# Performance work log

Hardware: AMD Instinct MI355X
Metric: run time of the kernel (lower is better)

The kernel has to match this reference:

```python
import jax, jax.numpy as jnp
import numpy as np

S, M, B, D, H, DH = 1024, 1024, 4, 1024, 16, 64
T = S + M
EPS = 1e-5


def setup_inputs() -> dict:
    key = jax.random.key(0)
    ks = jax.random.split(key, 6)
    x = jax.random.normal(ks[0], (S, B, D), dtype=jnp.float32)
    pos_emb = jax.random.normal(ks[1], (S, 1, D), dtype=jnp.float32)
    memory = jax.random.normal(ks[2], (M, B, D), dtype=jnp.float32)
    # causal mask: query i (global position M+i) cannot attend to key j > M+i
    i = jnp.arange(S)[:, None]
    j = jnp.arange(T)[None, :]
    mask = jnp.broadcast_to((j > (i + M))[:, :, None], (S, T, B))  # [S,T,B] bool
    w_qkv = jax.random.normal(ks[3], (D, 3 * H * DH), dtype=jnp.float32) * (D ** -0.5)
    w_o = jax.random.normal(ks[4], (H * DH, D), dtype=jnp.float32) * ((H * DH) ** -0.5)
    ln_gamma = jnp.ones((D,), dtype=jnp.float32)
    ln_beta = jnp.zeros((D,), dtype=jnp.float32)
    return {"x": x, "pos_emb": pos_emb, "memory": memory, "mask": mask,
            "w_qkv": w_qkv, "w_o": w_o, "ln_gamma": ln_gamma, "ln_beta": ln_beta}


def reference(x, pos_emb, memory, mask, w_qkv, w_o, ln_gamma, ln_beta):
    seq_len = x.shape[0]
    scale = 1.0 / (DH ** 0.5)
    x = x + pos_emb[-seq_len:]                      # [S,B,D]
    c = jnp.concatenate([memory, x], axis=0)        # [T,B,D]
    qkv = jnp.einsum('tbd,de->tbe', c, w_qkv)       # [T,B,3*H*DH]
    q, k, v = jnp.split(qkv, 3, axis=-1)
    q = q.reshape(-1, B, H, DH)[-seq_len:]          # [S,B,H,DH]
    k = k.reshape(-1, B, H, DH)                     # [T,B,H,DH]
    v = v.reshape(-1, B, H, DH)
    score = jnp.einsum('ibnd,jbnd->ijbn', q, k) * scale  # [S,T,B,H]
    score = jnp.where(mask[:, :, :, None], -jnp.inf, score)
    prob = jax.nn.softmax(score, axis=1)
    vec = jnp.einsum('ijbn,jbnd->ibnd', prob, v)    # [S,B,H,DH]
    vec = vec.reshape(seq_len, B, H * DH)
    attn_out = jnp.einsum('sbe,ed->sbd', vec, w_o)  # [S,B,D]
    y = x + attn_out
    mu = jnp.mean(y, axis=-1, keepdims=True)
    var = jnp.mean(jnp.square(y - mu), axis=-1, keepdims=True)
    out = (y - mu) * jax.lax.rsqrt(var + EPS) * ln_gamma + ln_beta
    return out
```

## Files before the change

### kernel.cpp

```cpp
#include <hip/hip_runtime.h>
#include <stdint.h>

#define S_  1024
#define M_  1024
#define B_  4
#define D_  1024
#define H_  16
#define DH_ 64
#define T_  2048

typedef __attribute__((ext_vector_type(8))) short bf8;
typedef __attribute__((ext_vector_type(4))) float f32x4;
typedef __attribute__((ext_vector_type(16))) float f32x16;
typedef __attribute__((ext_vector_type(8))) unsigned short u16x8;
typedef __attribute__((ext_vector_type(4))) unsigned short u16x4;
typedef __attribute__((ext_vector_type(4))) unsigned int u32x4;
typedef unsigned short u16;

#define MFMA(a, b, c)   __builtin_amdgcn_mfma_f32_16x16x32_bf16((a), (b), (c), 0, 0, 0)
#define MFMA32(a, b, c) __builtin_amdgcn_mfma_f32_32x32x16_bf16((a), (b), (c), 0, 0, 0)

#define SIG(r) ((((r) >> 1) ^ ((r) >> 3)) & 3)

static __device__ __forceinline__ u16 f2bf(float f) {
  unsigned int u = __builtin_bit_cast(unsigned int, f);
  u += 0x7fffu + ((u >> 16) & 1u);
  return (u16)(u >> 16);
}

static __device__ __forceinline__ void gload16(const void* g, void* l) {
  __builtin_amdgcn_global_load_lds((const __attribute__((address_space(1))) unsigned int*)g,
                                   (__attribute__((address_space(3))) unsigned int*)l,
                                   16, 0, 0);
}

static __device__ __forceinline__ float fexp2(float x) {
  return __builtin_amdgcn_exp2f(x);
}
static __device__ __forceinline__ unsigned int cvtpk(float lo, float hi) {
  unsigned int r; asm("v_cvt_pk_bf16_f32 %0, %1, %2" : "=v"(r) : "v"(lo), "v"(hi)); return r;
}
static __device__ __forceinline__ void plswap(unsigned int& a, unsigned int& b) {
  asm volatile("s_nop 1\n\tv_permlane32_swap_b32 %0, %1" : "+v"(a), "+v"(b));
}

__global__ __launch_bounds__(256) void k_prep(const float* __restrict__ x,
    const float* __restrict__ pos, const float* __restrict__ mem,
    u16* __restrict__ cbf, float* __restrict__ xp)
{
  const int gid = blockIdx.x * 256 + threadIdx.x;
  const int e = gid * 8;
  const int row = e >> 10, col = e & 1023;
  float4 v0, v1;
  if (e < M_ * B_ * D_) {
    v0 = *(const float4*)(mem + e);
    v1 = *(const float4*)(mem + e + 4);
  } else {
    const int i2 = e - M_ * B_ * D_;
    v0 = *(const float4*)(x + i2);
    v1 = *(const float4*)(x + i2 + 4);
    const int srow = i2 >> 12;
    const float4 p0 = *(const float4*)(pos + srow * 1024 + col);
    const float4 p1 = *(const float4*)(pos + srow * 1024 + col + 4);
    v0.x += p0.x; v0.y += p0.y; v0.z += p0.z; v0.w += p0.w;
    v1.x += p1.x; v1.y += p1.y; v1.z += p1.z; v1.w += p1.w;
    *(float4*)(xp + i2) = v0;
    *(float4*)(xp + i2 + 4) = v1;
  }
  u16x8 c;
  c[0] = f2bf(v0.x); c[1] = f2bf(v0.y); c[2] = f2bf(v0.z); c[3] = f2bf(v0.w);
  c[4] = f2bf(v1.x); c[5] = f2bf(v1.y); c[6] = f2bf(v1.z); c[7] = f2bf(v1.w);
  const int ch = col >> 3;
  const int chs = (ch & ~3) | ((ch & 3) ^ SIG(row));
  *(u16x8*)(cbf + (size_t)row * 1024 + chs * 8) = c;
}

__global__ __launch_bounds__(256) void k_wtrans(const float* __restrict__ src,
    u16* __restrict__ dst, int Rr, int Cc, int swz)
{
  __shared__ float tl[64][65];
  const int r0 = blockIdx.x * 64, c0 = blockIdx.y * 64;
  const int tid = threadIdx.x;
  const int lr = tid >> 4, lc = (tid & 15) * 4;
  for (int i = 0; i < 4; ++i) {
    const int rr = lr + i * 16;
    const float4 v = *(const float4*)(src + (size_t)(r0 + rr) * Cc + c0 + lc);
    tl[rr][lc] = v.x; tl[rr][lc + 1] = v.y; tl[rr][lc + 2] = v.z; tl[rr][lc + 3] = v.w;
  }
  __syncthreads();
  const int c = tid >> 2, k0 = (tid & 3) * 16;
  u16x8 a, b;
  for (int j = 0; j < 8; ++j) { a[j] = f2bf(tl[k0 + j][c]); b[j] = f2bf(tl[k0 + 8 + j][c]); }
  const int roww = c0 + c;
  int ch0 = (r0 + k0) >> 3, ch1 = ((r0 + k0) >> 3) + 1;
  if (swz) {
    const int sx = SIG(roww);
    ch0 = (ch0 & ~3) | ((ch0 & 3) ^ sx);
    ch1 = (ch1 & ~3) | ((ch1 & 3) ^ sx);
  }
  u16* dp = dst + (size_t)roww * Rr;
  *(u16x8*)(dp + ch0 * 8) = a;
  *(u16x8*)(dp + ch1 * 8) = b;
}

__global__ __launch_bounds__(256, 3) void k_gemm_qkvs(const u16* __restrict__ A,
    const u16* __restrict__ Bt, u16* __restrict__ Qd, u16* __restrict__ Kd,
    u16* __restrict__ VTd)
{
  __shared__ u16 sA[3][4096];
  __shared__ u16 sB[3][4096];
  const int tid = threadIdx.x, lane = tid & 63, wave = tid >> 6;
  const int lrow = lane & 15, lgrp = lane >> 4;
  const int wm = (wave >> 1) * 64, wn = (wave & 1) * 64;
  const int sr = lane >> 2, sk = (lane & 3) * 8;

  const int bid = blockIdx.x;
  const int lid = (bid & 7) * 160 + (bid >> 3);
  int rowb, colb;
  if (lid < 512) { rowb = lid >> 4; colb = 8 + (lid & 15); }
  else { const int l2 = lid - 512; const int q = l2 / 24; rowb = 32 + q; colb = l2 - q * 24; }
  const int row0 = rowb * 128, col0 = colb * 128;

  f32x4 acc[4][4];
#pragma unroll
  for (int i = 0; i < 4; ++i)
#pragma unroll
    for (int j = 0; j < 4; ++j) acc[i][j] = f32x4{0.f, 0.f, 0.f, 0.f};

#define STAGE_S(bufi, kt) do { const int k0_ = (kt) * 32;                      \
    _Pragma("unroll") for (int s_ = 0; s_ < 2; ++s_) {                         \
      const int rr_ = (wave * 2 + s_) * 16 + sr;                               \
      gload16(A + (size_t)(row0 + rr_) * 1024 + k0_ + sk,                      \
              &sA[bufi][(wave * 2 + s_) * 512]);                               \
      gload16(Bt + (size_t)(col0 + rr_) * 1024 + k0_ + sk,                     \
              &sB[bufi][(wave * 2 + s_) * 512]);                               \
    } } while (0)

  STAGE_S(0, 0); STAGE_S(1, 1);

  int c0 = 0;
#pragma unroll 1
  for (int t = 0; t < 32; ++t) {
    if (t < 31) { asm volatile("s_waitcnt vmcnt(4)" ::: "memory"); }
    else        { asm volatile("s_waitcnt vmcnt(0)" ::: "memory"); }
    __builtin_amdgcn_s_barrier();
    __builtin_amdgcn_sched_barrier(0);
    const int c2 = (c0 + 2 >= 3) ? c0 - 1 : c0 + 2;
    if (t <= 29) STAGE_S(c2, t + 2);
    bf8 af[4], bfv[4];
#pragma unroll
    for (int i = 0; i < 4; ++i) {
      const int r_ = wm + i * 16 + lrow;
      af[i] = *(const bf8*)&sA[c0][r_ * 32 + ((lgrp ^ SIG(r_)) << 3)];
    }
#pragma unroll
    for (int j = 0; j < 4; ++j) {
      const int r_ = wn + j * 16 + lrow;
      bfv[j] = *(const bf8*)&sB[c0][r_ * 32 + ((lgrp ^ SIG(r_)) << 3)];
    }
    __builtin_amdgcn_s_setprio(1);
#pragma unroll
    for (int i = 0; i < 4; ++i)
#pragma unroll
      for (int j = 0; j < 4; ++j) acc[i][j] = MFMA(af[i], bfv[j], acc[i][j]);
    __builtin_amdgcn_s_setprio(0);
    c0 = (c0 == 2) ? 0 : c0 + 1;
  }

  const int which = col0 >> 10;
#pragma unroll
  for (int i = 0; i < 4; ++i)
#pragma unroll
    for (int j = 0; j < 4; ++j)
#pragma unroll
      for (int r = 0; r < 4; ++r) {
        const int grow = row0 + wm + i * 16 + lgrp * 4 + r;
        const int gcol = col0 + wn + j * 16 + lrow;
        const u16 bv = f2bf(acc[i][j][r]);
        const int t = grow >> 2, bb2 = grow & 3;
        const int rem = gcol & 1023;
        const int bh = bb2 * 16 + (rem >> 6), dh = rem & 63;
        if (which == 0) {
          if (t >= M_) Qd[((size_t)bh * S_ + (t - M_)) * 64 + dh] = bv;
        } else if (which == 1) {
          Kd[((size_t)bh * T_ + t) * 64 + (dh ^ ((t & 7) << 3))] = bv;
        } else {
          VTd[((size_t)bh * 64 + dh) * T_ + (t & ~63) + ((t & 63) ^ ((dh & 7) << 3))] = bv;
        }
      }
}

__global__ __launch_bounds__(256) void k_gemm_out(const u16* __restrict__ A,
    const u16* __restrict__ Bt, const float* __restrict__ xp,
    float* __restrict__ y)
{
  __shared__ u16 sA[2][2048];
  __shared__ u16 sB[2][4096];
  const int tid = threadIdx.x, lane = tid & 63, wave = tid >> 6;
  const int lrow = lane & 15, lgrp = lane >> 4;
  const int wm = (wave >> 1) * 32, wn = (wave & 1) * 64;
  const int row0 = blockIdx.y * 64, col0 = blockIdx.x * 128;
  const int sr = lane >> 2, sk = (lane & 3) * 8;

  f32x4 acc[2][4];
  for (int i = 0; i < 2; ++i)
    for (int j = 0; j < 4; ++j) acc[i][j] = f32x4{0.f, 0.f, 0.f, 0.f};

#define STAGE_O(buf, kt) do { const int k0_ = (kt) * 32;                       \
    const int rra_ = wave * 16 + sr;                                           \
    gload16(A + (size_t)(row0 + rra_) * 1024 + k0_ + sk,                       \
            &sA[buf][wave * 512]);                                             \
    for (int s_ = 0; s_ < 2; ++s_) {                                           \
      const int rrb_ = (wave * 2 + s_) * 16 + sr;                              \
      gload16(Bt + (size_t)(col0 + rrb_) * 1024 + k0_ + sk,                    \
              &sB[buf][(wave * 2 + s_) * 512]);                                \
    } } while (0)

  STAGE_O(0, 0);
  int cur = 0;
  for (int kt = 0; kt < 32; ++kt) {
    asm volatile("s_waitcnt vmcnt(0)" ::: "memory");
    __syncthreads();
    if (kt + 1 < 32) STAGE_O(cur ^ 1, kt + 1);
    bf8 af[2], bfv[4];
    const u16* pa = &sA[cur][(wm + lrow) * 32 + lgrp * 8];
    const u16* pb = &sB[cur][(wn + lrow) * 32 + lgrp * 8];
    for (int i = 0; i < 2; ++i) af[i] = *(const bf8*)(pa + i * 512);
    for (int j = 0; j < 4; ++j) bfv[j] = *(const bf8*)(pb + j * 512);
    __builtin_amdgcn_s_setprio(1);
    for (int i = 0; i < 2; ++i)
      for (int j = 0; j < 4; ++j) acc[i][j] = MFMA(af[i], bfv[j], acc[i][j]);
    __builtin_amdgcn_s_setprio(0);
    cur ^= 1;
  }

  for (int i = 0; i < 2; ++i)
    for (int j = 0; j < 4; ++j)
      for (int r = 0; r < 4; ++r) {
        const int grow = row0 + wm + i * 16 + lgrp * 4 + r;
        const int gcol = col0 + wn + j * 16 + lrow;
        y[(size_t)grow * 1024 + gcol] = acc[i][j][r] + xp[(size_t)grow * 1024 + gcol];
      }
}

__global__ __launch_bounds__(256) void k_attn(const u16* __restrict__ Qd,
    const u16* __restrict__ Kd, const u16* __restrict__ VTd,
    u16* __restrict__ vec)
{
  __shared__ u16 Kl[2][4096];
  __shared__ u16 Vl[2][4096];
  const int tid = threadIdx.x, lane = tid & 63, wave = tid >> 6;
  const int ql = lane & 31, hi = lane >> 5;
  const int qb = blockIdx.x, bh = blockIdx.y;
  const int bb = bh >> 4, hh = bh & 15;
  const int q0 = qb * 128 + wave * 32;
  const int myq = q0 + ql;
  const int klim = M_ + myq;

  bf8 qf[4];
  const u16* qrow = Qd + ((size_t)bh * S_ + myq) * 64 + hi * 8;
#pragma unroll
  for (int c = 0; c < 4; ++c) qf[c] = *(const bf8*)(qrow + c * 16);

  const u16* kb = Kd + (size_t)bh * T_ * 64;
  const u16* vb = VTd + (size_t)bh * 64 * T_;

  f32x16 o0, o1;
#pragma unroll
  for (int r = 0; r < 16; ++r) { o0[r] = 0.f; o1[r] = 0.f; }
  float m_run = 0.f, l_run = 0.f;
  const float cs = 0.125f * 1.44269504f;

  const int nkt = (M_ + qb * 128 + 128) >> 6;

  auto stage = [&](int buf, int kt) {
    const int t0 = kt * 64;
#pragma unroll
    for (int i = 0; i < 2; ++i) {
      const int ch = i * 256 + tid;
      gload16(kb + (size_t)t0 * 64 + ch * 8, &Kl[buf][ch * 8]);
    }
#pragma unroll
    for (int i = 0; i < 2; ++i) {
      const int ch = i * 256 + tid;
      gload16(vb + (size_t)(ch >> 3) * T_ + t0 + (ch & 7) * 8, &Vl[buf][ch * 8]);
    }
  };

  stage(0, 0);
  int cur = 0;
  for (int kt = 0; kt < nkt; ++kt) {
    if (kt + 1 < nkt) {
      stage(cur ^ 1, kt + 1);
      asm volatile("s_waitcnt vmcnt(4)" ::: "memory");
    } else {
      asm volatile("s_waitcnt vmcnt(0)" ::: "memory");
    }
    __builtin_amdgcn_s_barrier();

    const u16* Kc = Kl[cur];
    const u16* Vc = Vl[cur];

    f32x16 s0, s1;
#pragma unroll
    for (int r = 0; r < 16; ++r) { s0[r] = 0.f; s1[r] = 0.f; }
    const int tr0 = ql, tr1 = 32 + ql;
    const int sw0 = (tr0 & 7) << 3;
    __builtin_amdgcn_s_setprio(1);
#pragma unroll
    for (int c = 0; c < 4; ++c) {
      const int db = c * 16 + hi * 8;
      const bf8 ka = *(const bf8*)(Kc + tr0 * 64 + (db ^ sw0));
      const bf8 kbfr = *(const bf8*)(Kc + tr1 * 64 + (db ^ sw0));
      s0 = MFMA32(ka, qf[c], s0);
      s1 = MFMA32(kbfr, qf[c], s1);
    }
    __builtin_amdgcn_s_setprio(0);

    float p0[16], p1[16];
#pragma unroll
    for (int r = 0; r < 16; ++r) { p0[r] = s0[r] * cs; p1[r] = s1[r] * cs; }
    if (kt * 64 + 63 > M_ + q0) {
#pragma unroll
      for (int r = 0; r < 16; ++r) {
        const int kg = kt * 64 + (r & 3) + 8 * (r >> 2) + 4 * hi;
        if (kg > klim)      p0[r] = -1e30f;
        if (kg + 32 > klim) p1[r] = -1e30f;
      }
    }
    float mx = fmaxf(p0[0], p1[0]);
#pragma unroll
    for (int r = 1; r < 16; ++r) mx = fmaxf(mx, fmaxf(p0[r], p1[r]));
    mx = fmaxf(mx, __shfl_xor(mx, 32));
    if (__any(mx - m_run > 8.f)) {
      const float mnew = fmaxf(m_run, mx);
      const float al = fexp2(m_run - mnew);
      l_run *= al;
#pragma unroll
      for (int r = 0; r < 16; ++r) {
        const int qloc = (r & 3) + 8 * (r >> 2) + 4 * hi;
        const float ar = __shfl(al, (lane & 32) + qloc);
        o0[r] *= ar; o1[r] *= ar;
      }
      m_run = mnew;
    }
    float rs = 0.f;
#pragma unroll
    for (int r = 0; r < 16; ++r) {
      p0[r] = fexp2(p0[r] - m_run);
      p1[r] = fexp2(p1[r] - m_run);
      rs += p0[r] + p1[r];
    }
    rs += __shfl_xor(rs, 32);
    l_run += rs;

    bf8 paf[2][2];
    {
      unsigned int a0 = cvtpk(p0[0], p0[1]),  a1 = cvtpk(p0[2], p0[3]);
      unsigned int a2 = cvtpk(p0[4], p0[5]),  a3 = cvtpk(p0[6], p0[7]);
      unsigned int b0 = cvtpk(p0[8], p0[9]),  b1 = cvtpk(p0[10], p0[11]);
      unsigned int b2 = cvtpk(p0[12], p0[13]), b3 = cvtpk(p0[14], p0[15]);
      plswap(a0, a2); plswap(a1, a3); plswap(b0, b2); plswap(b1, b3);
      u32x4 f0 = {a0, a1, a2, a3}, f1 = {b0, b1, b2, b3};
      paf[0][0] = __builtin_bit_cast(bf8, f0);
      paf[0][1] = __builtin_bit_cast(bf8, f1);
    }
    {
      unsigned int a0 = cvtpk(p1[0], p1[1]),  a1 = cvtpk(p1[2], p1[3]);
      unsigned int a2 = cvtpk(p1[4], p1[5]),  a3 = cvtpk(p1[6], p1[7]);
      unsigned int b0 = cvtpk(p1[8], p1[9]),  b1 = cvtpk(p1[10], p1[11]);
      unsigned int b2 = cvtpk(p1[12], p1[13]), b3 = cvtpk(p1[14], p1[15]);
      plswap(a0, a2); plswap(a1, a3); plswap(b0, b2); plswap(b1, b3);
      u32x4 f0 = {a0, a1, a2, a3}, f1 = {b0, b1, b2, b3};
      paf[1][0] = __builtin_bit_cast(bf8, f0);
      paf[1][1] = __builtin_bit_cast(bf8, f1);
    }

    __builtin_amdgcn_s_setprio(1);
#pragma unroll
    for (int kc = 0; kc < 4; ++kc) {
      const int tb = kc * 16 + hi * 8;
      const bf8 pfrag = paf[kc >> 1][kc & 1];
      const int vr0 = ql, vr1 = 32 + ql;
      const bf8 vf0 = *(const bf8*)(Vc + vr0 * 64 + (tb ^ ((vr0 & 7) << 3)));
      const bf8 vf1 = *(const bf8*)(Vc + vr1 * 64 + (tb ^ ((vr1 & 7) << 3)));
      o0 = MFMA32(pfrag, vf0, o0);
      o1 = MFMA32(pfrag, vf1, o1);
    }
    __builtin_amdgcn_s_setprio(0);
    __builtin_amdgcn_s_barrier();
    cur ^= 1;
  }

  const float linv = 1.0f / l_run;
#pragma unroll
  for (int r = 0; r < 16; ++r) {
    const int qloc = (r & 3) + 8 * (r >> 2) + 4 * hi;
    const float li = __shfl(linv, (lane & 32) + qloc);
    const int srow = q0 + qloc;
    const size_t base = ((size_t)srow * B_ + bb) * 1024 + hh * 64;
    vec[base + ql]      = f2bf(o0[r] * li);
    vec[base + 32 + ql] = f2bf(o1[r] * li);
  }
}

__global__ __launch_bounds__(256) void k_ln(const float* __restrict__ y,
    const float* __restrict__ g, const float* __restrict__ be,
    float* __restrict__ out)
{
  const int row = blockIdx.x, tid = threadIdx.x;
  const float4 v = *(const float4*)(y + (size_t)row * 1024 + tid * 4);
  float s = v.x + v.y + v.z + v.w;
  float ss = v.x * v.x + v.y * v.y + v.z * v.z + v.w * v.w;
  for (int mk = 1; mk < 64; mk <<= 1) { s += __shfl_xor(s, mk); ss += __shfl_xor(ss, mk); }
  __shared__ float red[8];
  if ((tid & 63) == 0) { red[tid >> 6] = s; red[4 + (tid >> 6)] = ss; }
  __syncthreads();
  s = red[0] + red[1] + red[2] + red[3];
  ss = red[4] + red[5] + red[6] + red[7];
  const float mu = s * (1.0f / 1024.0f);
  const float var = ss * (1.0f / 1024.0f) - mu * mu;
  const float rstd = rsqrtf(var + 1e-5f);
  const float4 gg = *(const float4*)(g + tid * 4);
  const float4 bb = *(const float4*)(be + tid * 4);
  float4 o;
  o.x = (v.x - mu) * rstd * gg.x + bb.x;
  o.y = (v.y - mu) * rstd * gg.y + bb.y;
  o.z = (v.z - mu) * rstd * gg.z + bb.z;
  o.w = (v.w - mu) * rstd * gg.w + bb.w;
  *(float4*)(out + (size_t)row * 1024 + tid * 4) = o;
}

extern "C" void kernel_launch(void* const* d_in, const int* in_sizes, int n_in,
                              void* d_out, int out_size, void* d_ws, size_t ws_size,
                              hipStream_t stream)
{
  const float* x     = (const float*)d_in[0];
  const float* pos   = (const float*)d_in[1];
  const float* mem   = (const float*)d_in[2];
  const float* wqkv  = (const float*)d_in[4];
  const float* wo    = (const float*)d_in[5];
  const float* gamma = (const float*)d_in[6];
  const float* beta  = (const float*)d_in[7];
  float* out = (float*)d_out;

  if (ws_size < ((size_t)104 << 20)) return;

  char* ws = (char*)d_ws;
  u16*   cbf = (u16*)(ws + 0);
  float* y   = (float*)(ws + 0);
  float* xp  = (float*)(ws + ((size_t)16 << 20));
  u16*   wqt = (u16*)(ws + ((size_t)32 << 20));
  u16*   wot = (u16*)(ws + ((size_t)38 << 20));
  u16*   Qd  = (u16*)(ws + ((size_t)40 << 20));
  u16*   Kd  = (u16*)(ws + ((size_t)48 << 20));
  u16*   VTd = (u16*)(ws + ((size_t)80 << 20));
  u16*   vec = (u16*)(ws + ((size_t)96 << 20));

  k_prep<<<4096, 256, 0, stream>>>(x, pos, mem, cbf, xp);
  k_wtrans<<<dim3(16, 48), 256, 0, stream>>>(wqkv, wqt, 1024, 3072, 1);
  k_wtrans<<<dim3(16, 16), 256, 0, stream>>>(wo, wot, 1024, 1024, 0);
  k_gemm_qkvs<<<1280, 256, 0, stream>>>(cbf, wqt, Qd, Kd, VTd);
  k_attn<<<dim3(8, 64), 256, 0, stream>>>(Qd, Kd, VTd, vec);
  k_gemm_out<<<dim3(8, 64), 256, 0, stream>>>(vec, wot, xp, y);
  k_ln<<<4096, 256, 0, stream>>>(y, gamma, beta, out);
}
```

Measured before the change: 199.6 us.

## Widen QKV GEMM tiles to 128x256 with 512 threads and remap attention blocks

The QKV projection GEMM now uses 512-thread blocks computing 128x256 output tiles with 8 waves, so each A tile is reused across twice as many columns. The old three-stage pipeline with a partial vmcnt wait becomes a two-stage double buffer with a full wait each step. Separately, the attention launch becomes 1D and block IDs are remapped (bid&7 stride) so blocks that share a batch-head land near each other across XCDs for better K/V cache reuse. The shallower pipeline may expose more load latency, and the larger blocks lower occupancy.

```diff
diff --git a/kernel.cpp b/kernel.cpp
--- a/kernel.cpp
+++ b/kernel.cpp
@@ -103,23 +103,22 @@
   *(u16x8*)(dp + ch1 * 8) = b;
 }
 
-__global__ __launch_bounds__(256, 3) void k_gemm_qkvs(const u16* __restrict__ A,
+__global__ __launch_bounds__(512, 2) void k_gemm_qkvw(const u16* __restrict__ A,
     const u16* __restrict__ Bt, u16* __restrict__ Qd, u16* __restrict__ Kd,
     u16* __restrict__ VTd)
 {
-  __shared__ u16 sA[3][4096];
-  __shared__ u16 sB[3][4096];
+  __shared__ u16 sA[2][4096];
+  __shared__ u16 sB[2][8192];
   const int tid = threadIdx.x, lane = tid & 63, wave = tid >> 6;
   const int lrow = lane & 15, lgrp = lane >> 4;
-  const int wm = (wave >> 1) * 64, wn = (wave & 1) * 64;
-  const int sr = lane >> 2, sk = (lane & 3) * 8;
+  const int wm = (wave >> 2) * 64, wn = (wave & 3) * 64;
 
   const int bid = blockIdx.x;
-  const int lid = (bid & 7) * 160 + (bid >> 3);
+  const int lid = (bid & 7) * 80 + (bid >> 3);
   int rowb, colb;
-  if (lid < 512) { rowb = lid >> 4; colb = 8 + (lid & 15); }
-  else { const int l2 = lid - 512; const int q = l2 / 24; rowb = 32 + q; colb = l2 - q * 24; }
-  const int row0 = rowb * 128, col0 = colb * 128;
+  if (lid < 128) { rowb = 32 + (lid >> 2); colb = lid & 3; }
+  else { const int l2 = lid - 128; rowb = l2 >> 3; colb = 4 + (l2 & 7); }
+  const int row0 = rowb * 128, col0 = colb * 256;
 
   f32x4 acc[4][4];
 #pragma unroll
@@ -127,36 +126,33 @@
 #pragma unroll
     for (int j = 0; j < 4; ++j) acc[i][j] = f32x4{0.f, 0.f, 0.f, 0.f};
 
-#define STAGE_S(bufi, kt) do { const int k0_ = (kt) * 32;                      \
+#define STAGE_W(bufi, kt) do { const int k0_ = (kt) * 32;                      \
+    { const int ca_ = tid;                                                     \
+      gload16(A + (size_t)(row0 + (ca_ >> 2)) * 1024 + k0_ + (ca_ & 3) * 8,    \
+              &sA[bufi][wave * 512]); }                                        \
     _Pragma("unroll") for (int s_ = 0; s_ < 2; ++s_) {                         \
-      const int rr_ = (wave * 2 + s_) * 16 + sr;                               \
-      gload16(A + (size_t)(row0 + rr_) * 1024 + k0_ + sk,                      \
-              &sA[bufi][(wave * 2 + s_) * 512]);                               \
-      gload16(Bt + (size_t)(col0 + rr_) * 1024 + k0_ + sk,                     \
-              &sB[bufi][(wave * 2 + s_) * 512]);                               \
+      const int cb_ = tid + s_ * 512;                                          \
+      gload16(Bt + (size_t)(col0 + (cb_ >> 2)) * 1024 + k0_ + (cb_ & 3) * 8,   \
+              &sB[bufi][s_ * 4096 + wave * 512]);                              \
     } } while (0)
 
-  STAGE_S(0, 0); STAGE_S(1, 1);
-
-  int c0 = 0;
+  STAGE_W(0, 0);
+  int cur = 0;
 #pragma unroll 1
-  for (int t = 0; t < 32; ++t) {
-    if (t < 31) { asm volatile("s_waitcnt vmcnt(4)" ::: "memory"); }
-    else        { asm volatile("s_waitcnt vmcnt(0)" ::: "memory"); }
-    __builtin_amdgcn_s_barrier();
-    __builtin_amdgcn_sched_barrier(0);
-    const int c2 = (c0 + 2 >= 3) ? c0 - 1 : c0 + 2;
-    if (t <= 29) STAGE_S(c2, t + 2);
+  for (int kt = 0; kt < 32; ++kt) {
+    asm volatile("s_waitcnt vmcnt(0)" ::: "memory");
+    __syncthreads();
+    if (kt + 1 < 32) STAGE_W(cur ^ 1, kt + 1);
     bf8 af[4], bfv[4];
 #pragma unroll
     for (int i = 0; i < 4; ++i) {
       const int r_ = wm + i * 16 + lrow;
-      af[i] = *(const bf8*)&sA[c0][r_ * 32 + ((lgrp ^ SIG(r_)) << 3)];
+      af[i] = *(const bf8*)&sA[cur][r_ * 32 + ((lgrp ^ SIG(r_)) << 3)];
     }
 #pragma unroll
     for (int j = 0; j < 4; ++j) {
       const int r_ = wn + j * 16 + lrow;
-      bfv[j] = *(const bf8*)&sB[c0][r_ * 32 + ((lgrp ^ SIG(r_)) << 3)];
+      bfv[j] = *(const bf8*)&sB[cur][r_ * 32 + ((lgrp ^ SIG(r_)) << 3)];
     }
     __builtin_amdgcn_s_setprio(1);
 #pragma unroll
@@ -164,7 +160,7 @@
 #pragma unroll
       for (int j = 0; j < 4; ++j) acc[i][j] = MFMA(af[i], bfv[j], acc[i][j]);
     __builtin_amdgcn_s_setprio(0);
-    c0 = (c0 == 2) ? 0 : c0 + 1;
+    cur ^= 1;
   }
 
   const int which = col0 >> 10;
@@ -251,7 +247,9 @@
   __shared__ u16 Vl[2][4096];
   const int tid = threadIdx.x, lane = tid & 63, wave = tid >> 6;
   const int ql = lane & 31, hi = lane >> 5;
-  const int qb = blockIdx.x, bh = blockIdx.y;
+  const int bid = blockIdx.x;
+  const int sw = (bid & 7) * 64 + (bid >> 3);
+  const int bh = sw >> 3, qb = sw & 7;
   const int bb = bh >> 4, hh = bh & 15;
   const int q0 = qb * 128 + wave * 32;
   const int myq = q0 + ql;
@@ -460,8 +458,8 @@
   k_prep<<<4096, 256, 0, stream>>>(x, pos, mem, cbf, xp);
   k_wtrans<<<dim3(16, 48), 256, 0, stream>>>(wqkv, wqt, 1024, 3072, 1);
   k_wtrans<<<dim3(16, 16), 256, 0, stream>>>(wo, wot, 1024, 1024, 0);
-  k_gemm_qkvs<<<1280, 256, 0, stream>>>(cbf, wqt, Qd, Kd, VTd);
-  k_attn<<<dim3(8, 64), 256, 0, stream>>>(Qd, Kd, VTd, vec);
+  k_gemm_qkvw<<<640, 512, 0, stream>>>(cbf, wqt, Qd, Kd, VTd);
+  k_attn<<<512, 256, 0, stream>>>(Qd, Kd, VTd, vec);
   k_gemm_out<<<dim3(8, 64), 256, 0, stream>>>(vec, wot, xp, y);
   k_ln<<<4096, 256, 0, stream>>>(y, gamma, beta, out);
 }
```

Result: no change. 198.9 us (-0.3%).
